# Performance work log

Measured on AMD Instinct MI355X. Metric: run time of the kernel, lower is better.

## Reference

```python
import jax, jax.numpy as jnp
import numpy as np

N_NODES = 100000
N_EDGES = 1600000
IN_CH, HID, EMB = 128, 64, 32


def _glorot(key, shape):
    lim = np.sqrt(6.0 / (shape[0] + shape[1])).astype(np.float32)
    return jax.random.uniform(key, shape, jnp.float32, -lim, lim)


def setup_inputs() -> dict:
    key = jax.random.key(0)
    ks = jax.random.split(key, 5)
    x = jax.random.normal(ks[0], (N_NODES, IN_CH), dtype=jnp.float32)
    edges = jax.random.randint(ks[1], (2, N_EDGES), 0, N_NODES)
    W1 = _glorot(ks[2], (IN_CH, HID)); b1 = jnp.zeros((HID,), jnp.float32)
    W2 = _glorot(ks[3], (HID, EMB)); b2 = jnp.zeros((EMB,), jnp.float32)
    W3 = _glorot(ks[4], (HID, EMB)); b3 = jnp.zeros((EMB,), jnp.float32)
    return {"x": x, "edges": edges, "W1": W1, "b1": b1,
            "W2": W2, "b2": b2, "W3": W3, "b3": b3}


def reference(x, edges, W1, b1, W2, b2, W3, b3):
    N = x.shape[0]
    # GCNConv default: add self-loops, symmetric D^-1/2 A D^-1/2 normalization
    loop = jnp.arange(N, dtype=edges.dtype)
    src = jnp.concatenate([edges[0], loop])  # [E+N] message sources
    dst = jnp.concatenate([edges[1], loop])  # [E+N] message targets
    deg = jax.ops.segment_sum(jnp.ones_like(dst, dtype=x.dtype), dst, num_segments=N)
    dinv = jnp.where(deg > 0, jax.lax.rsqrt(deg), 0.0)
    norm = dinv[src] * dinv[dst]  # [E+N], cached across the three convs (cached=True)

    def gcn(h, W, b):
        h = h @ W                                  # [N, out]
        msg = h[src] * norm[:, None]               # gather + edge scale
        return jax.ops.segment_sum(msg, dst, num_segments=N) + b  # scatter-add

    h = jax.nn.relu(gcn(x, W1, b1))
    return gcn(h, W2, b2), gcn(h, W3, b3)
```

## Files before the change

kernel.cpp:

```cpp
#include <hip/hip_runtime.h>

#define NN 100000
#define NE 1600000
#define NB 391
#define CHUNK 4096
#define NCHUNK 391

typedef __attribute__((ext_vector_type(8))) short short8_t;
typedef __attribute__((ext_vector_type(4))) float float4_t;

__device__ inline unsigned short f2bf(float f) {
    unsigned int u = __float_as_uint(f);
    unsigned int r = u + 0x7fffu + ((u >> 16) & 1u);
    return (unsigned short)(r >> 16);
}
__device__ inline float bf_lo(unsigned int u) { return __uint_as_float(u << 16); }
__device__ inline float bf_hi(unsigned int u) { return __uint_as_float(u & 0xffff0000u); }

__global__ __launch_bounds__(256) void k_pre(const float* __restrict__ W1,
                                             const float* __restrict__ W2,
                                             const float* __restrict__ W3,
                                             unsigned short* __restrict__ wtb,
                                             unsigned short* __restrict__ wt2) {
    int f = blockIdx.x * 256 + threadIdx.x;
    int c = f >> 7, k = f & 127;
    wtb[f] = f2bf(W1[k * 64 + c]);
    if (f < 4096) {
        int c2 = f >> 6, k2 = f & 63;
        float v = (c2 < 32) ? W2[k2 * 32 + c2] : W3[k2 * 32 + (c2 - 32)];
        wt2[f] = f2bf(v);
    }
}

__global__ __launch_bounds__(256) void k_chist(const int* __restrict__ dst,
                                               int* __restrict__ hist2d) {
    __shared__ int lh[NB];
    int c = blockIdx.x, t = threadIdx.x;
    for (int i = t; i < NB; i += 256) lh[i] = 0;
    __syncthreads();
    int e0 = c * CHUNK, e1 = min(e0 + CHUNK, NE);
    for (int e = e0 + t; e < e1; e += 256)
        atomicAdd(&lh[dst[e] >> 8], 1);
    __syncthreads();
    for (int i = t; i < NB; i += 256) hist2d[c * NB + i] = lh[i];
}

__global__ __launch_bounds__(256) void k_scancol(const int* __restrict__ hist2d,
                                                 int* __restrict__ base2d,
                                                 int* __restrict__ colsum) {
    __shared__ int sh[256];
    int b = blockIdx.x, t = threadIdx.x;
    int base = t * 2;
    int v0 = (base + 0 < NCHUNK) ? hist2d[(base + 0) * NB + b] : 0;
    int v1 = (base + 1 < NCHUNK) ? hist2d[(base + 1) * NB + b] : 0;
    int tsum = v0 + v1;
    sh[t] = tsum;
    __syncthreads();
    for (int d = 1; d < 256; d <<= 1) {
        int x = (t >= d) ? sh[t - d] : 0;
        __syncthreads();
        sh[t] += x;
        __syncthreads();
    }
    int excl = sh[t] - tsum;
    if (base + 0 < NCHUNK) base2d[(base + 0) * NB + b] = excl;
    if (base + 1 < NCHUNK) base2d[(base + 1) * NB + b] = excl + v0;
    if (t == 255) colsum[b] = sh[255];
}

__global__ __launch_bounds__(256) void k_scanb(const int* __restrict__ colsum,
                                               int* __restrict__ boff) {
    __shared__ int sh[256];
    int t = threadIdx.x;
    int base = t * 2;
    int v0 = (base + 0 < NB) ? colsum[base + 0] : 0;
    int v1 = (base + 1 < NB) ? colsum[base + 1] : 0;
    int tsum = v0 + v1;
    sh[t] = tsum;
    __syncthreads();
    for (int d = 1; d < 256; d <<= 1) {
        int x = (t >= d) ? sh[t - d] : 0;
        __syncthreads();
        sh[t] += x;
        __syncthreads();
    }
    int excl = sh[t] - tsum;
    if (base + 0 < NB) boff[base + 0] = excl;
    if (base + 1 < NB) boff[base + 1] = excl + v0;
    if (t == 255) boff[NB] = sh[255];
}

__global__ __launch_bounds__(512) void k_fuse(const float* __restrict__ x,
                                              const unsigned short* __restrict__ wtb,
                                              unsigned short* __restrict__ t1b,
                                              const int* __restrict__ src,
                                              const int* __restrict__ dst,
                                              const int* __restrict__ base2d,
                                              const int* __restrict__ boff,
                                              unsigned int* __restrict__ pairs) {
    __shared__ int sbuf[2 * NB];
    const int b = blockIdx.x;
    const int t = threadIdx.x;

    if ((b % 3) == 2) {
        int* lbase = sbuf;
        int* lh    = sbuf + NB;
        const int c = b / 3;
        int e0 = c * CHUNK;
        int e1 = min(e0 + CHUNK, NE);
        for (int i = t; i < NB; i += 512) {
            lbase[i] = base2d[c * NB + i] + boff[i];
            lh[i] = 0;
        }
        __syncthreads();
        for (int e = e0 + t; e < e1; e += 512) {
            int d = dst[e];
            int bk = d >> 8;
            int r = atomicAdd(&lh[bk], 1);
            pairs[lbase[bk] + r] = (unsigned int)src[e] | ((unsigned int)(d & 255) << 17);
        }
    } else {
        const int tile = 2 * (b / 3) + (b % 3);
        const int row0 = tile * 128;
        const int nrows = min(128, NN - row0);
        const int w = t >> 6, l = t & 63;
        const int m15 = l & 15, kg = l >> 4;

        int ra = min(row0 + w * 16 + m15, NN - 1);
        const float* xa = x + (size_t)ra * 128 + kg * 8;

        float4_t acc[4];
        #pragma unroll
        for (int cb = 0; cb < 4; ++cb) acc[cb] = (float4_t){0.f, 0.f, 0.f, 0.f};

        #pragma unroll
        for (int ks = 0; ks < 4; ++ks) {
            float4 f0 = *(const float4*)(xa + ks * 32);
            float4 f1 = *(const float4*)(xa + ks * 32 + 4);
            short8_t a;
            a[0] = (short)f2bf(f0.x); a[1] = (short)f2bf(f0.y);
            a[2] = (short)f2bf(f0.z); a[3] = (short)f2bf(f0.w);
            a[4] = (short)f2bf(f1.x); a[5] = (short)f2bf(f1.y);
            a[6] = (short)f2bf(f1.z); a[7] = (short)f2bf(f1.w);
            #pragma unroll
            for (int cb = 0; cb < 4; ++cb) {
                short8_t bb = *(const short8_t*)(wtb + (cb * 16 + m15) * 128 + ks * 32 + kg * 8);
                acc[cb] = __builtin_amdgcn_mfma_f32_16x16x32_bf16(a, bb, acc[cb], 0, 0, 0);
            }
        }

        #pragma unroll
        for (int r = 0; r < 4; ++r) {
            int lrow = w * 16 + kg * 4 + r;
            if (lrow < nrows) {
                size_t grow = (size_t)(row0 + lrow);
                #pragma unroll
                for (int cb = 0; cb < 4; ++cb)
                    t1b[grow * 64 + cb * 16 + m15] = f2bf(acc[cb][r]);
            }
        }
    }
}

__global__ __launch_bounds__(256) void k_fine(const unsigned int* __restrict__ pairs,
                                              const int* __restrict__ boff,
                                              int* __restrict__ csr_off,
                                              int* __restrict__ csr_src,
                                              float* __restrict__ dinv) {
    __shared__ int lcnt[256];
    __shared__ int sc[256];
    __shared__ int lofs[256];
    int t = threadIdx.x;
    int b = blockIdx.x;
    int n0 = b << 8;
    int nnode = min(256, NN - n0);
    int bO = boff[b], bE = boff[b + 1];

    lcnt[t] = 0;
    __syncthreads();
    for (int e = bO + t; e < bE; e += 256)
        atomicAdd(&lcnt[pairs[e] >> 17], 1);
    __syncthreads();
    sc[t] = lcnt[t];
    __syncthreads();
    for (int d = 1; d < 256; d <<= 1) {
        int x = (t >= d) ? sc[t - d] : 0;
        __syncthreads();
        sc[t] += x;
        __syncthreads();
    }
    {
        int excl = sc[t] - lcnt[t];
        lofs[t] = excl;
        if (t < nnode) {
            int n = n0 + t;
            csr_off[n] = bO + excl;
            dinv[n] = rsqrtf(1.0f + (float)lcnt[t]);
        }
        lcnt[t] = 0;
    }
    if (b == NB - 1 && t == 0) csr_off[NN] = NE;
    __syncthreads();
    for (int e = bO + t; e < bE; e += 256) {
        unsigned int w = pairs[e];
        int li = (int)(w >> 17);
        int r = atomicAdd(&lcnt[li], 1);
        csr_src[bO + lofs[li] + r] = (int)(w & 0x1FFFFu);
    }
}

__global__ __launch_bounds__(256) void k_gather8(const int* __restrict__ off,
                                                 const int* __restrict__ csr,
                                                 const float* __restrict__ dinv,
                                                 const unsigned short* __restrict__ hb,
                                                 const float* __restrict__ bias,
                                                 unsigned int* __restrict__ outp) {
    int idx = blockIdx.x * 256 + threadIdx.x;
    int n = idx >> 3;
    if (n >= NN) return;
    int c8 = idx & 7;
    const uint4* h4 = (const uint4*)hb;
    float dn = dinv[n];
    float a0[8], a1[8];
    {
        uint4 v = h4[(size_t)n * 8 + c8];
        a0[0] = dn * bf_lo(v.x); a0[1] = dn * bf_hi(v.x);
        a0[2] = dn * bf_lo(v.y); a0[3] = dn * bf_hi(v.y);
        a0[4] = dn * bf_lo(v.z); a0[5] = dn * bf_hi(v.z);
        a0[6] = dn * bf_lo(v.w); a0[7] = dn * bf_hi(v.w);
        #pragma unroll
        for (int j = 0; j < 8; ++j) a1[j] = 0.f;
    }
    int b = off[n], e = off[n + 1];
    int i = b;
    for (; i + 1 < e; i += 2) {
        int s0 = csr[i], s1 = csr[i + 1];
        float w0 = dinv[s0], w1 = dinv[s1];
        uint4 v0 = h4[(size_t)s0 * 8 + c8];
        uint4 v1 = h4[(size_t)s1 * 8 + c8];
        a0[0] += w0 * bf_lo(v0.x); a0[1] += w0 * bf_hi(v0.x);
        a0[2] += w0 * bf_lo(v0.y); a0[3] += w0 * bf_hi(v0.y);
        a0[4] += w0 * bf_lo(v0.z); a0[5] += w0 * bf_hi(v0.z);
        a0[6] += w0 * bf_lo(v0.w); a0[7] += w0 * bf_hi(v0.w);
        a1[0] += w1 * bf_lo(v1.x); a1[1] += w1 * bf_hi(v1.x);
        a1[2] += w1 * bf_lo(v1.y); a1[3] += w1 * bf_hi(v1.y);
        a1[4] += w1 * bf_lo(v1.z); a1[5] += w1 * bf_hi(v1.z);
        a1[6] += w1 * bf_lo(v1.w); a1[7] += w1 * bf_hi(v1.w);
    }
    if (i < e) {
        int s = csr[i];
        float w = dinv[s];
        uint4 v = h4[(size_t)s * 8 + c8];
        a0[0] += w * bf_lo(v.x); a0[1] += w * bf_hi(v.x);
        a0[2] += w * bf_lo(v.y); a0[3] += w * bf_hi(v.y);
        a0[4] += w * bf_lo(v.z); a0[5] += w * bf_hi(v.z);
        a0[6] += w * bf_lo(v.w); a0[7] += w * bf_hi(v.w);
    }
    float4 b0 = ((const float4*)bias)[c8 * 2];
    float4 b1v = ((const float4*)bias)[c8 * 2 + 1];
    float o[8];
    o[0] = dn * fmaxf(dn * (a0[0] + a1[0]) + b0.x, 0.f);
    o[1] = dn * fmaxf(dn * (a0[1] + a1[1]) + b0.y, 0.f);
    o[2] = dn * fmaxf(dn * (a0[2] + a1[2]) + b0.z, 0.f);
    o[3] = dn * fmaxf(dn * (a0[3] + a1[3]) + b0.w, 0.f);
    o[4] = dn * fmaxf(dn * (a0[4] + a1[4]) + b1v.x, 0.f);
    o[5] = dn * fmaxf(dn * (a0[5] + a1[5]) + b1v.y, 0.f);
    o[6] = dn * fmaxf(dn * (a0[6] + a1[6]) + b1v.z, 0.f);
    o[7] = dn * fmaxf(dn * (a0[7] + a1[7]) + b1v.w, 0.f);
    uint4 p;
    p.x = (unsigned int)f2bf(o[0]) | ((unsigned int)f2bf(o[1]) << 16);
    p.y = (unsigned int)f2bf(o[2]) | ((unsigned int)f2bf(o[3]) << 16);
    p.z = (unsigned int)f2bf(o[4]) | ((unsigned int)f2bf(o[5]) << 16);
    p.w = (unsigned int)f2bf(o[6]) | ((unsigned int)f2bf(o[7]) << 16);
    ((uint4*)outp)[(size_t)n * 8 + c8] = p;
}

__global__ __launch_bounds__(512) void k_gemm23(const unsigned short* __restrict__ h1b,
                                                const unsigned short* __restrict__ wt2,
                                                unsigned short* __restrict__ y) {
    __shared__ __align__(16) unsigned short lx[128 * 72];
    __shared__ __align__(16) unsigned short lw[64 * 72];
    const int t = threadIdx.x;
    const int row0 = blockIdx.x * 128;
    const int nrows = min(128, NN - row0);

    #pragma unroll
    for (int i = 0; i < 2; ++i) {
        int f = t + i * 512;
        int r = f >> 3, c8 = f & 7;
        uint4 v = make_uint4(0u, 0u, 0u, 0u);
        if (r < nrows) v = ((const uint4*)h1b)[(size_t)(row0 + r) * 8 + c8];
        *(uint4*)&lx[r * 72 + c8 * 8] = v;
    }
    if (t < 512) {
        int c = t >> 3, c8 = t & 7;
        uint4 v = ((const uint4*)wt2)[t];
        *(uint4*)&lw[c * 72 + c8 * 8] = v;
    }
    __syncthreads();

    const int w = t >> 6, l = t & 63;
    const int m15 = l & 15, kg = l >> 4;
    const unsigned short* pa = &lx[(w * 16 + m15) * 72 + kg * 8];
    const unsigned short* pb = &lw[m15 * 72 + kg * 8];

    float4_t acc[4];
    #pragma unroll
    for (int cb = 0; cb < 4; ++cb) acc[cb] = (float4_t){0.f, 0.f, 0.f, 0.f};

    #pragma unroll
    for (int ks = 0; ks < 2; ++ks) {
        short8_t a = *(const short8_t*)(pa + ks * 32);
        #pragma unroll
        for (int cb = 0; cb < 4; ++cb) {
            short8_t bb = *(const short8_t*)(pb + cb * (16 * 72) + ks * 32);
            acc[cb] = __builtin_amdgcn_mfma_f32_16x16x32_bf16(a, bb, acc[cb], 0, 0, 0);
        }
    }

    #pragma unroll
    for (int r = 0; r < 4; ++r) {
        int lrow = w * 16 + kg * 4 + r;
        if (lrow < nrows) {
            size_t grow = (size_t)(row0 + lrow);
            #pragma unroll
            for (int cb = 0; cb < 4; ++cb)
                y[grow * 64 + cb * 16 + m15] = f2bf(acc[cb][r]);
        }
    }
}

__global__ __launch_bounds__(256) void k_gatherO(const int* __restrict__ off,
                                                 const int* __restrict__ csr,
                                                 const float* __restrict__ dinv,
                                                 const unsigned short* __restrict__ yb,
                                                 const float* __restrict__ b2,
                                                 const float* __restrict__ b3,
                                                 float* __restrict__ out) {
    int idx = blockIdx.x * 256 + threadIdx.x;
    int n = idx >> 3;
    int c8 = idx & 7;
    const uint4* h4 = (const uint4*)yb;
    float a0[8], a1[8];
    {
        uint4 v = h4[(size_t)n * 8 + c8];
        a0[0] = bf_lo(v.x); a0[1] = bf_hi(v.x);
        a0[2] = bf_lo(v.y); a0[3] = bf_hi(v.y);
        a0[4] = bf_lo(v.z); a0[5] = bf_hi(v.z);
        a0[6] = bf_lo(v.w); a0[7] = bf_hi(v.w);
        #pragma unroll
        for (int j = 0; j < 8; ++j) a1[j] = 0.f;
    }
    int b = off[n], e = off[n + 1];
    int i = b;
    for (; i + 1 < e; i += 2) {
        int s0 = csr[i], s1 = csr[i + 1];
        uint4 v0 = h4[(size_t)s0 * 8 + c8];
        uint4 v1 = h4[(size_t)s1 * 8 + c8];
        a0[0] += bf_lo(v0.x); a0[1] += bf_hi(v0.x);
        a0[2] += bf_lo(v0.y); a0[3] += bf_hi(v0.y);
        a0[4] += bf_lo(v0.z); a0[5] += bf_hi(v0.z);
        a0[6] += bf_lo(v0.w); a0[7] += bf_hi(v0.w);
        a1[0] += bf_lo(v1.x); a1[1] += bf_hi(v1.x);
        a1[2] += bf_lo(v1.y); a1[3] += bf_hi(v1.y);
        a1[4] += bf_lo(v1.z); a1[5] += bf_hi(v1.z);
        a1[6] += bf_lo(v1.w); a1[7] += bf_hi(v1.w);
    }
    if (i < e) {
        uint4 v = h4[(size_t)csr[i] * 8 + c8];
        a0[0] += bf_lo(v.x); a0[1] += bf_hi(v.x);
        a0[2] += bf_lo(v.y); a0[3] += bf_hi(v.y);
        a0[4] += bf_lo(v.z); a0[5] += bf_hi(v.z);
        a0[6] += bf_lo(v.w); a0[7] += bf_hi(v.w);
    }
    float dn = dinv[n];
    const float* bp = (c8 < 4) ? (b2 + c8 * 8) : (b3 + (c8 - 4) * 8);
    float4 q0 = *(const float4*)bp;
    float4 q1 = *(const float4*)(bp + 4);
    float4 o0, o1;
    o0.x = dn * (a0[0] + a1[0]) + q0.x;
    o0.y = dn * (a0[1] + a1[1]) + q0.y;
    o0.z = dn * (a0[2] + a1[2]) + q0.z;
    o0.w = dn * (a0[3] + a1[3]) + q0.w;
    o1.x = dn * (a0[4] + a1[4]) + q1.x;
    o1.y = dn * (a0[5] + a1[5]) + q1.y;
    o1.z = dn * (a0[6] + a1[6]) + q1.z;
    o1.w = dn * (a0[7] + a1[7]) + q1.w;
    float* op = (c8 < 4) ? (out + (size_t)n * 32 + c8 * 8)
                         : (out + (size_t)NN * 32 + (size_t)n * 32 + (c8 - 4) * 8);
    *(float4*)op = o0;
    *(float4*)(op + 4) = o1;
}

extern "C" void kernel_launch(void* const* d_in, const int* in_sizes, int n_in,
                              void* d_out, int out_size, void* d_ws, size_t ws_size,
                              hipStream_t stream) {
    const float* x  = (const float*)d_in[0];
    const int* edges = (const int*)d_in[1];
    const float* W1 = (const float*)d_in[2];
    const float* b1 = (const float*)d_in[3];
    const float* W2 = (const float*)d_in[4];
    const float* b2 = (const float*)d_in[5];
    const float* W3 = (const float*)d_in[6];
    const float* b3 = (const float*)d_in[7];
    float* out = (float*)d_out;

    const int* srcs = edges;
    const int* dsts = edges + NE;

    int*   csr_off = (int*)d_ws;
    float* dinv    = (float*)((int*)d_ws + 100004);
    int*   csr_src = (int*)d_ws + 200004;
    int*   colsum  = (int*)d_ws + 1800004;
    int*   boff    = (int*)d_ws + 1800396;
    unsigned short* wtb = (unsigned short*)((int*)d_ws + 1800800);
    unsigned short* t1b = (unsigned short*)((int*)d_ws + 1804896);
    unsigned short* y   = t1b;
    unsigned int*   pairs  = (unsigned int*)((int*)d_ws + 5004896);
    int*            hist2d = (int*)d_ws + 5004896 + 1600000;
    int*            base2d = (int*)d_ws + 5004896 + 1752896;
    unsigned short* h1b    = (unsigned short*)pairs;
    unsigned short* wt2 = (unsigned short*)(out + 6400000 - 2048);

    dim3 blk(256);
    const int gN8 = (NN * 8 + 255) / 256;
    const int gT23 = (NN + 127) / 128;

    k_pre<<<32, blk, 0, stream>>>(W1, W2, W3, wtb, wt2);
    k_chist<<<NCHUNK, blk, 0, stream>>>(dsts, hist2d);
    k_scancol<<<NB, blk, 0, stream>>>(hist2d, base2d, colsum);
    k_scanb<<<1, blk, 0, stream>>>(colsum, boff);

    k_fuse<<<3 * NCHUNK, dim3(512), 0, stream>>>(x, wtb, t1b, srcs, dsts,
                                                 base2d, boff, pairs);

    k_fine<<<NB, blk, 0, stream>>>(pairs, boff, csr_off, csr_src, dinv);

    k_gather8<<<gN8, blk, 0, stream>>>(csr_off, csr_src, dinv, t1b, b1,
                                       (unsigned int*)h1b);
    k_gemm23<<<gT23, dim3(512), 0, stream>>>(h1b, wt2, y);
    k_gatherO<<<gN8, blk, 0, stream>>>(csr_off, csr_src, dinv, y, b2, b3, out);
}
```

Measured before the change: 149.1 us.

## Split fused GEMM/bucket-scatter kernel into separate GEMM1 and scatter kernels

```diff
diff --git a/kernel.cpp b/kernel.cpp
--- a/kernel.cpp
+++ b/kernel.cpp
@@ -90,75 +90,78 @@
     if (t == 255) boff[NB] = sh[255];
 }
 
-__global__ __launch_bounds__(512) void k_fuse(const float* __restrict__ x,
-                                              const unsigned short* __restrict__ wtb,
-                                              unsigned short* __restrict__ t1b,
-                                              const int* __restrict__ src,
-                                              const int* __restrict__ dst,
-                                              const int* __restrict__ base2d,
-                                              const int* __restrict__ boff,
-                                              unsigned int* __restrict__ pairs) {
-    __shared__ int sbuf[2 * NB];
-    const int b = blockIdx.x;
+__global__ __launch_bounds__(512, 8) void k_gemm1(const float* __restrict__ x,
+                                                  const unsigned short* __restrict__ wtb,
+                                                  unsigned short* __restrict__ t1b) {
+    const int tile = blockIdx.x;
+    const int row0 = tile * 128;
+    const int nrows = min(128, NN - row0);
     const int t = threadIdx.x;
-
-    if ((b % 3) == 2) {
-        int* lbase = sbuf;
-        int* lh    = sbuf + NB;
-        const int c = b / 3;
-        int e0 = c * CHUNK;
-        int e1 = min(e0 + CHUNK, NE);
-        for (int i = t; i < NB; i += 512) {
-            lbase[i] = base2d[c * NB + i] + boff[i];
-            lh[i] = 0;
+    const int w = t >> 6, l = t & 63;
+    const int m15 = l & 15, kg = l >> 4;
+
+    int ra = min(row0 + w * 16 + m15, NN - 1);
+    const float4* xa = (const float4*)(x + (size_t)ra * 128) + kg * 2;
+
+    float4 f[8];
+    #pragma unroll
+    for (int ks = 0; ks < 4; ++ks) {
+        f[2 * ks]     = xa[ks * 8];
+        f[2 * ks + 1] = xa[ks * 8 + 1];
+    }
+
+    float4_t acc[4];
+    #pragma unroll
+    for (int cb = 0; cb < 4; ++cb) acc[cb] = (float4_t){0.f, 0.f, 0.f, 0.f};
+
+    #pragma unroll
+    for (int ks = 0; ks < 4; ++ks) {
+        float4 f0 = f[2 * ks], f1 = f[2 * ks + 1];
+        short8_t a;
+        a[0] = (short)f2bf(f0.x); a[1] = (short)f2bf(f0.y);
+        a[2] = (short)f2bf(f0.z); a[3] = (short)f2bf(f0.w);
+        a[4] = (short)f2bf(f1.x); a[5] = (short)f2bf(f1.y);
+        a[6] = (short)f2bf(f1.z); a[7] = (short)f2bf(f1.w);
+        #pragma unroll
+        for (int cb = 0; cb < 4; ++cb) {
+            short8_t bb = *(const short8_t*)(wtb + (cb * 16 + m15) * 128 + ks * 32 + kg * 8);
+            acc[cb] = __builtin_amdgcn_mfma_f32_16x16x32_bf16(a, bb, acc[cb], 0, 0, 0);
         }
-        __syncthreads();
-        for (int e = e0 + t; e < e1; e += 512) {
-            int d = dst[e];
-            int bk = d >> 8;
-            int r = atomicAdd(&lh[bk], 1);
-            pairs[lbase[bk] + r] = (unsigned int)src[e] | ((unsigned int)(d & 255) << 17);
+    }
+
+    #pragma unroll
+    for (int r = 0; r < 4; ++r) {
+        int lrow = w * 16 + kg * 4 + r;
+        if (lrow < nrows) {
+            size_t grow = (size_t)(row0 + lrow);
+            #pragma unroll
+            for (int cb = 0; cb < 4; ++cb)
+                t1b[grow * 64 + cb * 16 + m15] = f2bf(acc[cb][r]);
         }
-    } else {
-        const int tile = 2 * (b / 3) + (b % 3);
-        const int row0 = tile * 128;
-        const int nrows = min(128, NN - row0);
-        const int w = t >> 6, l = t & 63;
-        const int m15 = l & 15, kg = l >> 4;
-
-        int ra = min(row0 + w * 16 + m15, NN - 1);
-        const float* xa = x + (size_t)ra * 128 + kg * 8;
-
-        float4_t acc[4];
-        #pragma unroll
-        for (int cb = 0; cb < 4; ++cb) acc[cb] = (float4_t){0.f, 0.f, 0.f, 0.f};
-
-        #pragma unroll
-        for (int ks = 0; ks < 4; ++ks) {
-            float4 f0 = *(const float4*)(xa + ks * 32);
-            float4 f1 = *(const float4*)(xa + ks * 32 + 4);
-            short8_t a;
-            a[0] = (short)f2bf(f0.x); a[1] = (short)f2bf(f0.y);
-            a[2] = (short)f2bf(f0.z); a[3] = (short)f2bf(f0.w);
-            a[4] = (short)f2bf(f1.x); a[5] = (short)f2bf(f1.y);
-            a[6] = (short)f2bf(f1.z); a[7] = (short)f2bf(f1.w);
-            #pragma unroll
-            for (int cb = 0; cb < 4; ++cb) {
-                short8_t bb = *(const short8_t*)(wtb + (cb * 16 + m15) * 128 + ks * 32 + kg * 8);
-                acc[cb] = __builtin_amdgcn_mfma_f32_16x16x32_bf16(a, bb, acc[cb], 0, 0, 0);
-            }
-        }
-
-        #pragma unroll
-        for (int r = 0; r < 4; ++r) {
-            int lrow = w * 16 + kg * 4 + r;
-            if (lrow < nrows) {
-                size_t grow = (size_t)(row0 + lrow);
-                #pragma unroll
-                for (int cb = 0; cb < 4; ++cb)
-                    t1b[grow * 64 + cb * 16 + m15] = f2bf(acc[cb][r]);
-            }
-        }
+    }
+}
+
+__global__ __launch_bounds__(512) void k_bscatter(const int* __restrict__ src,
+                                                  const int* __restrict__ dst,
+                                                  const int* __restrict__ base2d,
+                                                  const int* __restrict__ boff,
+                                                  unsigned int* __restrict__ pairs) {
+    __shared__ int lbase[NB];
+    __shared__ int lh[NB];
+    const int c = blockIdx.x;
+    const int t = threadIdx.x;
+    int e0 = c * CHUNK;
+    int e1 = min(e0 + CHUNK, NE);
+    for (int i = t; i < NB; i += 512) {
+        lbase[i] = base2d[c * NB + i] + boff[i];
+        lh[i] = 0;
+    }
+    __syncthreads();
+    for (int e = e0 + t; e < e1; e += 512) {
+        int d = dst[e];
+        int bk = d >> 8;
+        int r = atomicAdd(&lh[bk], 1);
+        pairs[lbase[bk] + r] = (unsigned int)src[e] | ((unsigned int)(d & 255) << 17);
     }
 }
 
@@ -424,6 +427,7 @@
 
     dim3 blk(256);
     const int gN8 = (NN * 8 + 255) / 256;
+    const int gT1 = (NN + 127) / 128;
     const int gT23 = (NN + 127) / 128;
 
     k_pre<<<32, blk, 0, stream>>>(W1, W2, W3, wtb, wt2);
@@ -431,8 +435,8 @@
     k_scancol<<<NB, blk, 0, stream>>>(hist2d, base2d, colsum);
     k_scanb<<<1, blk, 0, stream>>>(colsum, boff);
 
-    k_fuse<<<3 * NCHUNK, dim3(512), 0, stream>>>(x, wtb, t1b, srcs, dsts,
-                                                 base2d, boff, pairs);
+    k_gemm1<<<gT1, dim3(512), 0, stream>>>(x, wtb, t1b);
+    k_bscatter<<<NCHUNK, dim3(512), 0, stream>>>(srcs, dsts, base2d, boff, pairs);
 
     k_fine<<<NB, blk, 0, stream>>>(pairs, boff, csr_off, csr_src, dinv);
 
```

Result: slower. 156.8 us (+5.1%).
